# Kernel tuning notes

Measured on AMD Instinct MI355X. Metric: run time of the kernel, lower is better.

Reference implementation:

```python
import jax, jax.numpy as jnp
from jax import lax
import numpy as np

B, T, F_IN, H = 64, 128, 12, 128  # batch, seq_len, input/output features, hidden


def _uinit(key, shape, fan):
    return jax.random.uniform(key, shape, jnp.float32, -1.0, 1.0) / np.float32(np.sqrt(fan))


def setup_inputs() -> dict:
    key = jax.random.key(0)
    ks = jax.random.split(key, 12)
    inp = {
        "x": jax.random.normal(ks[0], (B, T, F_IN), jnp.float32),
        # encoder LSTM (gate order i,f,g,o; b = b_ih + b_hh folded together)
        "enc_Wih": _uinit(ks[1], (4 * H, F_IN), H),
        "enc_Whh": _uinit(ks[2], (4 * H, H), H),
        "enc_b": _uinit(ks[3], (4 * H,), H),
        # decoder LSTM (input is the 12-dim teacher-forced x slice)
        "dec_Wih": _uinit(ks[4], (4 * H, F_IN), H),
        "dec_Whh": _uinit(ks[5], (4 * H, H), H),
        "dec_b": _uinit(ks[6], (4 * H,), H),
        # attention: Linear(2H -> H) with bias, then v: Linear(H -> 1, no bias)
        "attn_W": _uinit(ks[7], (H, 2 * H), 2 * H),
        "attn_b": _uinit(ks[8], (H,), 2 * H),
        "v_w": _uinit(ks[9], (H,), H),
        # output layer: Linear(2H -> F_IN)  (intended width; see notes)
        "out_W": _uinit(ks[10], (F_IN, 2 * H), 2 * H),
        "out_b": _uinit(ks[11], (F_IN,), 2 * H),
    }
    return inp


def _lstm_cell(xt, h, c, Wih, Whh, b):
    z = xt @ Wih.T + h @ Whh.T + b  # [B, 4H]
    i, f, g, o = jnp.split(z, 4, axis=-1)
    c = jax.nn.sigmoid(f) * c + jax.nn.sigmoid(i) * jnp.tanh(g)
    h = jax.nn.sigmoid(o) * jnp.tanh(c)
    return h, c


def reference(x, enc_Wih, enc_Whh, enc_b, dec_Wih, dec_Whh, dec_b,
              attn_W, attn_b, v_w, out_W, out_b):
    b_, t_, _ = x.shape
    hdim = enc_Whh.shape[1]
    xs = jnp.swapaxes(x, 0, 1)  # [T, B, F]
    h0 = jnp.zeros((b_, hdim), x.dtype)
    c0 = jnp.zeros((b_, hdim), x.dtype)

    def enc_step(carry, xt):
        h, c = carry
        h, c = _lstm_cell(xt, h, c, enc_Wih, enc_Whh, enc_b)
        return (h, c), h

    (hT, cT), enc_hs = lax.scan(enc_step, (h0, c0), xs)
    enc_out = jnp.swapaxes(enc_hs, 0, 1)  # [B, T, H]

    # split attn weight: cat(hidden, enc_out) @ W.T == hidden@W1.T + enc_out@W2.T
    W1, W2 = attn_W[:, :hdim], attn_W[:, hdim:]
    enc_proj = jnp.einsum("bth,gh->btg", enc_out, W2)  # precompute encoder side

    def dec_step(carry, xt):
        h, c = carry
        h, c = _lstm_cell(xt, h, c, dec_Wih, dec_Whh, dec_b)
        energy = jnp.tanh((h @ W1.T)[:, None, :] + enc_proj + attn_b)  # [B,T,H]
        score = jnp.einsum("bth,h->bt", energy, v_w)
        w = jax.nn.softmax(score, axis=1)  # attention over encoder time
        ctx = jnp.einsum("bt,bth->bh", w, enc_out)
        return (h, c), jnp.concatenate([h, ctx], axis=-1)  # [B, 2H]

    _, dec_ys = lax.scan(dec_step, (hT, cT), xs)
    dec_out = jnp.swapaxes(dec_ys, 0, 1)  # [B, T, 2H]
    return dec_out @ out_W.T + out_b  # [B, T, F]
```

## Files before the change

### kernel.cpp

```cpp
#include <hip/hip_runtime.h>
#include <hip/hip_bf16.h>

#define BB 64
#define TT 128
#define FIN 12
#define HH 128
#define GG 512

#define LOG2E 1.4426950408889634f
#define TWO_LOG2E 2.8853900817779268f

__device__ __forceinline__ float fexp2(float x) { return __builtin_amdgcn_exp2f(x); }
__device__ __forceinline__ float frcp(float x)  { return __builtin_amdgcn_rcpf(x); }

__device__ __forceinline__ float tanh_f(float x) {
  return 1.0f - 2.0f * frcp(1.0f + fexp2(TWO_LOG2E * x));
}
__device__ __forceinline__ float sigm_f(float x) {
  return frcp(1.0f + fexp2(-LOG2E * x));
}

#define FMA4S(acc, s, v) do { \
  acc.x = fmaf((s), (v).x, acc.x); \
  acc.y = fmaf((s), (v).y, acc.y); \
  acc.z = fmaf((s), (v).z, acc.z); \
  acc.w = fmaf((s), (v).w, acc.w); } while (0)

__global__ __launch_bounds__(1024, 4) void lstm_kernel(
    const float* __restrict__ x,
    const float* __restrict__ eWih, const float* __restrict__ eWhh, const float* __restrict__ eb,
    const float* __restrict__ dWih, const float* __restrict__ dWhh, const float* __restrict__ db,
    float* __restrict__ encH, float* __restrict__ decH)
{
  const int b   = blockIdx.x;
  const int tid = threadIdx.x;
  const int g   = tid & 511;
  const int kh  = tid >> 9;

  __shared__ __align__(16) float xs[TT * FIN];
  __shared__ __align__(16) float h_lds[HH];
  __shared__ __align__(16) float part[2 * GG];

  if (tid < (TT * FIN / 4))
    ((float4*)xs)[tid] = ((const float4*)(x + (size_t)b * TT * FIN))[tid];
  if (tid < HH) h_lds[tid] = 0.0f;
  float c = 0.0f;

  #pragma unroll 1
  for (int phase = 0; phase < 2; ++phase) {
    const float* Wih  = phase ? dWih : eWih;
    const float* Whh  = phase ? dWhh : eWhh;
    const float* bias = phase ? db : eb;
    float* Hout       = phase ? decH : encH;

    float4 whh[16];
    #pragma unroll
    for (int j = 0; j < 16; ++j)
      whh[j] = *(const float4*)(Whh + g * HH + kh * 64 + 4 * j);
    float wih[6];
    #pragma unroll
    for (int j = 0; j < 6; ++j)
      wih[j] = Wih[g * FIN + kh * 6 + j];

    float b_i = 0.f, b_f = 0.f, b_g = 0.f, b_o = 0.f;
    if (tid < HH) {
      b_i = bias[tid];
      b_f = bias[HH + tid];
      b_g = bias[2 * HH + tid];
      b_o = bias[3 * HH + tid];
    }

    #pragma unroll 1
    for (int t = 0; t < TT; ++t) {
      __syncthreads();
      float a0, a1, a2 = 0.0f, a3 = 0.0f;
      {
        const float2* xt2 = (const float2*)(xs + t * FIN + kh * 6);
        float2 x0 = xt2[0], x1 = xt2[1], x2 = xt2[2];
        a0 = x0.x * wih[0]; a1 = x0.y * wih[1];
        a0 = fmaf(x1.x, wih[2], a0); a1 = fmaf(x1.y, wih[3], a1);
        a0 = fmaf(x2.x, wih[4], a0); a1 = fmaf(x2.y, wih[5], a1);
      }
      const float* hbase = h_lds + kh * 64;
      #pragma unroll
      for (int k = 0; k < 64; k += 4) {
        float4 h4 = *(const float4*)(hbase + k);
        a0 = fmaf(h4.x, whh[k >> 2].x, a0);
        a1 = fmaf(h4.y, whh[k >> 2].y, a1);
        a2 = fmaf(h4.z, whh[k >> 2].z, a2);
        a3 = fmaf(h4.w, whh[k >> 2].w, a3);
      }
      part[2 * g + kh] = (a0 + a1) + (a2 + a3);
      __syncthreads();
      if (tid < HH) {
        float2 pi = *(const float2*)&part[2 * tid];
        float2 pf = *(const float2*)&part[2 * (HH + tid)];
        float2 pg = *(const float2*)&part[2 * (2 * HH + tid)];
        float2 po = *(const float2*)&part[2 * (3 * HH + tid)];
        float zi = sigm_f(pi.x + pi.y + b_i);
        float zf = sigm_f(pf.x + pf.y + b_f);
        float zg = tanh_f(pg.x + pg.y + b_g);
        float zo = sigm_f(po.x + po.y + b_o);
        c = fmaf(zf, c, zi * zg);
        float hn = zo * tanh_f(c);
        h_lds[tid] = hn;
        Hout[((size_t)b * TT + t) * HH + tid] = hn;
      }
    }
  }
}

__global__ __launch_bounds__(256, 2) void proj_kernel(
    const float* __restrict__ encH, const float* __restrict__ decH,
    const float* __restrict__ attnW, const float* __restrict__ attnb,
    float* __restrict__ Abuf, float* __restrict__ Pbuf)
{
  const int m  = blockIdx.x & 1;
  const int b  = (blockIdx.x >> 1) & 63;
  const int r0 = (blockIdx.x >> 7) * 16;
  const int tid = threadIdx.x;

  __shared__ __align__(16) float WT[64 * 128];
  __shared__ __align__(16) float Xt[16 * 128];

  const float* X = (m ? encH : decH) + ((size_t)b * TT + r0) * HH;
  const float* W = attnW + (m ? HH : 0);

  ((float4*)Xt)[tid]       = ((const float4*)X)[tid];
  ((float4*)Xt)[256 + tid] = ((const float4*)X)[256 + tid];

  const int hq = tid & 31, rr = tid >> 5;
  const int h0 = 4 * hq;

  float4 acc0, acc1;
  if (m == 0) { acc0 = *(const float4*)(attnb + h0); acc1 = acc0; }
  else        { acc0 = make_float4(0.f, 0.f, 0.f, 0.f); acc1 = acc0; }

  for (int kb = 0; kb < 2; ++kb) {
    __syncthreads();
    {
      int h = tid >> 1, koff = (tid & 1) * 32;
      #pragma unroll
      for (int j = 0; j < 8; ++j) {
        float4 v = *(const float4*)(W + h * 256 + kb * 64 + koff + 4 * j);
        int kp = koff + 4 * j;
        WT[(kp + 0) * 128 + h] = v.x;
        WT[(kp + 1) * 128 + h] = v.y;
        WT[(kp + 2) * 128 + h] = v.z;
        WT[(kp + 3) * 128 + h] = v.w;
      }
    }
    __syncthreads();
    const float* xr0 = Xt + (2 * rr) * 128 + kb * 64;
    const float* xr1 = xr0 + 128;
    #pragma unroll
    for (int k4 = 0; k4 < 64; k4 += 4) {
      float4 xa = *(const float4*)(xr0 + k4);
      float4 xb = *(const float4*)(xr1 + k4);
      float4 w0 = *(const float4*)&WT[(k4 + 0) * 128 + h0];
      float4 w1 = *(const float4*)&WT[(k4 + 1) * 128 + h0];
      float4 w2 = *(const float4*)&WT[(k4 + 2) * 128 + h0];
      float4 w3 = *(const float4*)&WT[(k4 + 3) * 128 + h0];
      FMA4S(acc0, xa.x, w0); FMA4S(acc0, xa.y, w1);
      FMA4S(acc0, xa.z, w2); FMA4S(acc0, xa.w, w3);
      FMA4S(acc1, xb.x, w0); FMA4S(acc1, xb.y, w1);
      FMA4S(acc1, xb.z, w2); FMA4S(acc1, xb.w, w3);
    }
  }
  float* O = (m ? Pbuf : Abuf) + ((size_t)b * TT + r0) * HH;
  *(float4*)(O + (2 * rr) * 128 + h0)     = acc0;
  *(float4*)(O + (2 * rr + 1) * 128 + h0) = acc1;
}

__global__ __launch_bounds__(512, 2) void attn_kernel(
    const float* __restrict__ encH, const float* __restrict__ decH,
    const float* __restrict__ Abuf, const float* __restrict__ Pbuf,
    const float* __restrict__ vw, const float* __restrict__ outW,
    const float* __restrict__ outb, float* __restrict__ out)
{
  const int b  = blockIdx.x >> 3;
  const int s0 = (blockIdx.x & 7) * 16;
  const int tid = threadIdx.x;

  __shared__ __align__(16) float buf[64 * 128];
  __shared__ __align__(16) float a_lds[16 * 128];
  __shared__ __align__(16) float sc[16 * 128];
  __shared__ __align__(16) float dh[16 * 128];
  __shared__ __align__(16) float vl[HH];

  ((float4*)a_lds)[tid] = ((const float4*)(Abuf + ((size_t)b * TT + s0) * HH))[tid];
  ((float4*)dh)[tid]    = ((const float4*)(decH + ((size_t)b * TT + s0) * HH))[tid];
  if (tid < 32) ((float4*)vl)[tid] = ((const float4*)vw)[tid];

  const int u  = tid & 31;
  const int sl = tid >> 5;
  const int uq = u & 15;
  const int uh = u >> 4;

  for (int half = 0; half < 2; ++half) {
    const int tbase = half * 64;
    __syncthreads();
    #pragma unroll
    for (int i = 0; i < 4; ++i) {
      int flat = i * 2048 + tid * 4;
      int tp = flat >> 7;
      int h0 = flat & 127;
      float4 v = *(const float4*)(Pbuf + ((size_t)b * TT + tbase + tp) * HH + h0);
      int tq = tp >> 2, tr = tp & 3;
      buf[(h0 + 0) * 64 + 4 * ((tq ^ ((h0 + 0) >> 2)) & 15) + tr] = v.x;
      buf[(h0 + 1) * 64 + 4 * ((tq ^ ((h0 + 1) >> 2)) & 15) + tr] = v.y;
      buf[(h0 + 2) * 64 + 4 * ((tq ^ ((h0 + 2) >> 2)) & 15) + tr] = v.z;
      buf[(h0 + 3) * 64 + 4 * ((tq ^ ((h0 + 3) >> 2)) & 15) + tr] = v.w;
    }
    __syncthreads();
    float4 acc = make_float4(0.f, 0.f, 0.f, 0.f);
    const float* arow = a_lds + sl * 128;
    #pragma unroll 8
    for (int hh = 0; hh < 64; ++hh) {
      int h = uh * 64 + hh;
      float ah = arow[h];
      float vh = vl[h];
      float4 p4 = *(const float4*)&buf[h * 64 + 4 * ((uq ^ ((h >> 2) & 15)) & 15)];
      acc.x = fmaf(vh, tanh_f(ah + p4.x), acc.x);
      acc.y = fmaf(vh, tanh_f(ah + p4.y), acc.y);
      acc.z = fmaf(vh, tanh_f(ah + p4.z), acc.z);
      acc.w = fmaf(vh, tanh_f(ah + p4.w), acc.w);
    }
    acc.x += __shfl_xor(acc.x, 16, 64);
    acc.y += __shfl_xor(acc.y, 16, 64);
    acc.z += __shfl_xor(acc.z, 16, 64);
    acc.w += __shfl_xor(acc.w, 16, 64);
    if (uh == 0) *(float4*)&sc[sl * 128 + tbase + 4 * uq] = acc;
  }
  __syncthreads();

  {
    float4 sv = *(const float4*)&sc[sl * 128 + 4 * u];
    float mx = fmaxf(fmaxf(sv.x, sv.y), fmaxf(sv.z, sv.w));
    #pragma unroll
    for (int msk = 1; msk <= 16; msk <<= 1) mx = fmaxf(mx, __shfl_xor(mx, msk, 64));
    float4 e;
    e.x = fexp2(LOG2E * (sv.x - mx));
    e.y = fexp2(LOG2E * (sv.y - mx));
    e.z = fexp2(LOG2E * (sv.z - mx));
    e.w = fexp2(LOG2E * (sv.w - mx));
    float sm = (e.x + e.y) + (e.z + e.w);
    #pragma unroll
    for (int msk = 1; msk <= 16; msk <<= 1) sm += __shfl_xor(sm, msk, 64);
    float r = frcp(sm);
    e.x *= r; e.y *= r; e.z *= r; e.w *= r;
    *(float4*)&sc[sl * 128 + 4 * u] = e;
  }

  float4 ctx = make_float4(0.f, 0.f, 0.f, 0.f);
  const int h0c = 4 * u;
  for (int half = 0; half < 2; ++half) {
    const int tbase = half * 64;
    __syncthreads();
    #pragma unroll
    for (int i = 0; i < 4; ++i) {
      int flat = i * 2048 + tid * 4;
      int tp = flat >> 7;
      int hh0 = flat & 127;
      *(float4*)&buf[tp * 128 + hh0] =
          *(const float4*)(encH + ((size_t)b * TT + tbase + tp) * HH + hh0);
    }
    __syncthreads();
    const float* wrow = sc + sl * 128 + tbase;
    #pragma unroll 8
    for (int tp = 0; tp < 64; ++tp) {
      float wt = wrow[tp];
      float4 e4 = *(const float4*)&buf[tp * 128 + h0c];
      FMA4S(ctx, wt, e4);
    }
  }
  __syncthreads();
  *(float4*)&a_lds[sl * 128 + h0c] = ctx;
  __syncthreads();

  if (tid < 192) {
    int s = tid / 12, f = tid % 12;
    float acc = outb[f];
    const float4* w4 = (const float4*)(outW + f * 256);
    const float4* d4 = (const float4*)(dh + s * 128);
    const float4* c4 = (const float4*)(a_lds + s * 128);
    #pragma unroll
    for (int k = 0; k < 32; ++k) {
      float4 wv = w4[k], dv = d4[k];
      acc = fmaf(wv.x, dv.x, acc); acc = fmaf(wv.y, dv.y, acc);
      acc = fmaf(wv.z, dv.z, acc); acc = fmaf(wv.w, dv.w, acc);
    }
    #pragma unroll
    for (int k = 0; k < 32; ++k) {
      float4 wv = w4[32 + k], cv = c4[k];
      acc = fmaf(wv.x, cv.x, acc); acc = fmaf(wv.y, cv.y, acc);
      acc = fmaf(wv.z, cv.z, acc); acc = fmaf(wv.w, cv.w, acc);
    }
    out[((size_t)b * TT + s0 + s) * FIN + f] = acc;
  }
}

extern "C" void kernel_launch(void* const* d_in, const int* in_sizes, int n_in,
                              void* d_out, int out_size, void* d_ws, size_t ws_size,
                              hipStream_t stream)
{
  const float* x     = (const float*)d_in[0];
  const float* eWih  = (const float*)d_in[1];
  const float* eWhh  = (const float*)d_in[2];
  const float* eb    = (const float*)d_in[3];
  const float* dWih  = (const float*)d_in[4];
  const float* dWhh  = (const float*)d_in[5];
  const float* db    = (const float*)d_in[6];
  const float* attnW = (const float*)d_in[7];
  const float* attnb = (const float*)d_in[8];
  const float* vw    = (const float*)d_in[9];
  const float* outW  = (const float*)d_in[10];
  const float* outb  = (const float*)d_in[11];
  float* out = (float*)d_out;

  float* ws   = (float*)d_ws;
  const size_t SEG = (size_t)BB * TT * HH;
  float* encH = ws;
  float* decH = ws + SEG;
  float* Abuf = ws + 2 * SEG;
  float* Pbuf = ws + 3 * SEG;

  lstm_kernel<<<64, 1024, 0, stream>>>(x, eWih, eWhh, eb, dWih, dWhh, db, encH, decH);
  proj_kernel<<<1024, 256, 0, stream>>>(encH, decH, attnW, attnb, Abuf, Pbuf);
  attn_kernel<<<512, 512, 0, stream>>>(encH, decH, Abuf, Pbuf, vw, outW, outb, out);
}
```

Measured before the change: 391.0 us.

## Split LSTM gate dot products across 8-lane groups and reduce with shuffles

```diff
diff --git a/kernel.cpp b/kernel.cpp
--- a/kernel.cpp
+++ b/kernel.cpp
@@ -25,6 +25,10 @@
   acc.y = fmaf((s), (v).y, acc.y); \
   acc.z = fmaf((s), (v).z, acc.z); \
   acc.w = fmaf((s), (v).w, acc.w); } while (0)
+
+#define ACC4(hv, wv, a) do { \
+  a = fmaf((hv).x, (wv).x, a); a = fmaf((hv).y, (wv).y, a); \
+  a = fmaf((hv).z, (wv).z, a); a = fmaf((hv).w, (wv).w, a); } while (0)
 
 __global__ __launch_bounds__(1024, 4) void lstm_kernel(
     const float* __restrict__ x,
@@ -34,18 +38,21 @@
 {
   const int b   = blockIdx.x;
   const int tid = threadIdx.x;
-  const int g   = tid & 511;
-  const int kh  = tid >> 9;
+  const int q   = tid & 7;
+  const int i   = tid >> 3;
 
   __shared__ __align__(16) float xs[TT * FIN];
-  __shared__ __align__(16) float h_lds[HH];
-  __shared__ __align__(16) float part[2 * GG];
+  __shared__ __align__(16) float hbuf[2][160];
 
   if (tid < (TT * FIN / 4))
     ((float4*)xs)[tid] = ((const float4*)(x + (size_t)b * TT * FIN))[tid];
-  if (tid < HH) h_lds[tid] = 0.0f;
+  if (tid < 320) ((float*)hbuf)[tid] = 0.0f;
   float c = 0.0f;
 
+  const int xo   = (q < 4) ? 3 * q : 0;
+  const float xz = (q < 4) ? 1.0f : 0.0f;
+
+  int ts = 0;
   #pragma unroll 1
   for (int phase = 0; phase < 2; ++phase) {
     const float* Wih  = phase ? dWih : eWih;
@@ -53,58 +60,60 @@
     const float* bias = phase ? db : eb;
     float* Hout       = phase ? decH : encH;
 
-    float4 whh[16];
-    #pragma unroll
-    for (int j = 0; j < 16; ++j)
-      whh[j] = *(const float4*)(Whh + g * HH + kh * 64 + 4 * j);
-    float wih[6];
-    #pragma unroll
-    for (int j = 0; j < 6; ++j)
-      wih[j] = Wih[g * FIN + kh * 6 + j];
-
-    float b_i = 0.f, b_f = 0.f, b_g = 0.f, b_o = 0.f;
-    if (tid < HH) {
-      b_i = bias[tid];
-      b_f = bias[HH + tid];
-      b_g = bias[2 * HH + tid];
-      b_o = bias[3 * HH + tid];
-    }
+    float4 wg[4][4];
+    #pragma unroll
+    for (int g = 0; g < 4; ++g)
+      #pragma unroll
+      for (int j = 0; j < 4; ++j)
+        wg[g][j] = *(const float4*)(Whh + ((g * HH + i) * HH) + 16 * q + 4 * j);
+
+    float wx[4][3];
+    #pragma unroll
+    for (int g = 0; g < 4; ++g)
+      #pragma unroll
+      for (int j = 0; j < 3; ++j)
+        wx[g][j] = Wih[(g * HH + i) * FIN + xo + j] * xz;
+
+    const float bi = bias[i], bf = bias[HH + i], bg = bias[2 * HH + i], bo = bias[3 * HH + i];
 
     #pragma unroll 1
-    for (int t = 0; t < TT; ++t) {
+    for (int t = 0; t < TT; ++t, ++ts) {
       __syncthreads();
-      float a0, a1, a2 = 0.0f, a3 = 0.0f;
-      {
-        const float2* xt2 = (const float2*)(xs + t * FIN + kh * 6);
-        float2 x0 = xt2[0], x1 = xt2[1], x2 = xt2[2];
-        a0 = x0.x * wih[0]; a1 = x0.y * wih[1];
-        a0 = fmaf(x1.x, wih[2], a0); a1 = fmaf(x1.y, wih[3], a1);
-        a0 = fmaf(x2.x, wih[4], a0); a1 = fmaf(x2.y, wih[5], a1);
+      const float* hb = hbuf[ts & 1] + q * 20;
+      float4 h0 = *(const float4*)(hb + 0);
+      float4 h1 = *(const float4*)(hb + 4);
+      float4 h2 = *(const float4*)(hb + 8);
+      float4 h3 = *(const float4*)(hb + 12);
+
+      const float* xt = xs + t * FIN + xo;
+      float x0 = xt[0], x1 = xt[1], x2 = xt[2];
+      float ai = wx[0][0] * x0 + wx[0][1] * x1 + wx[0][2] * x2;
+      float af = wx[1][0] * x0 + wx[1][1] * x1 + wx[1][2] * x2;
+      float ag = wx[2][0] * x0 + wx[2][1] * x1 + wx[2][2] * x2;
+      float ao = wx[3][0] * x0 + wx[3][1] * x1 + wx[3][2] * x2;
+
+      ACC4(h0, wg[0][0], ai); ACC4(h0, wg[1][0], af); ACC4(h0, wg[2][0], ag); ACC4(h0, wg[3][0], ao);
+      ACC4(h1, wg[0][1], ai); ACC4(h1, wg[1][1], af); ACC4(h1, wg[2][1], ag); ACC4(h1, wg[3][1], ao);
+      ACC4(h2, wg[0][2], ai); ACC4(h2, wg[1][2], af); ACC4(h2, wg[2][2], ag); ACC4(h2, wg[3][2], ao);
+      ACC4(h3, wg[0][3], ai); ACC4(h3, wg[1][3], af); ACC4(h3, wg[2][3], ag); ACC4(h3, wg[3][3], ao);
+
+      #pragma unroll
+      for (int m = 1; m <= 4; m <<= 1) {
+        ai += __shfl_xor(ai, m, 64);
+        af += __shfl_xor(af, m, 64);
+        ag += __shfl_xor(ag, m, 64);
+        ao += __shfl_xor(ao, m, 64);
       }
-      const float* hbase = h_lds + kh * 64;
-      #pragma unroll
-      for (int k = 0; k < 64; k += 4) {
-        float4 h4 = *(const float4*)(hbase + k);
-        a0 = fmaf(h4.x, whh[k >> 2].x, a0);
-        a1 = fmaf(h4.y, whh[k >> 2].y, a1);
-        a2 = fmaf(h4.z, whh[k >> 2].z, a2);
-        a3 = fmaf(h4.w, whh[k >> 2].w, a3);
-      }
-      part[2 * g + kh] = (a0 + a1) + (a2 + a3);
-      __syncthreads();
-      if (tid < HH) {
-        float2 pi = *(const float2*)&part[2 * tid];
-        float2 pf = *(const float2*)&part[2 * (HH + tid)];
-        float2 pg = *(const float2*)&part[2 * (2 * HH + tid)];
-        float2 po = *(const float2*)&part[2 * (3 * HH + tid)];
-        float zi = sigm_f(pi.x + pi.y + b_i);
-        float zf = sigm_f(pf.x + pf.y + b_f);
-        float zg = tanh_f(pg.x + pg.y + b_g);
-        float zo = sigm_f(po.x + po.y + b_o);
+
+      if (q == 0) {
+        float zi = sigm_f(ai + bi);
+        float zf = sigm_f(af + bf);
+        float zg = tanh_f(ag + bg);
+        float zo = sigm_f(ao + bo);
         c = fmaf(zf, c, zi * zg);
         float hn = zo * tanh_f(c);
-        h_lds[tid] = hn;
-        Hout[((size_t)b * TT + t) * HH + tid] = hn;
+        hbuf[(ts + 1) & 1][(i >> 4) * 20 + (i & 15)] = hn;
+        Hout[((size_t)b * TT + t) * HH + i] = hn;
       }
     }
   }
```

New measurement: 368.7 us. -5.7%, faster.
